# Kernel optimization log

Measured on AMD Instinct MI355X. Metric: run time of the kernel, lower is better.

Reference implementation:

```python
import jax, jax.numpy as jnp
import numpy as np

B, T, D, H = 2, 2048, 2048, 32
d = D // H  # head_dim = 64


def setup_inputs() -> dict:
    key = jax.random.key(0)
    ks = jax.random.split(key, 6)
    s = 2 ** (-2.5) * (2.0 / (D + D)) ** 0.5  # xavier_uniform-ish scale, gain 2^-2.5
    return {
        "hidden_states": jax.random.normal(ks[0], (B, T, D), jnp.float32),
        "Wq": jax.random.normal(ks[1], (D, D), jnp.float32) * s,
        "Wk": jax.random.normal(ks[2], (D, D), jnp.float32) * s,
        "Wv": jax.random.normal(ks[3], (D, D), jnp.float32) * s,
        "Wbeta": jax.random.normal(ks[4], (D, H), jnp.float32) * s,
        "b_beta": jnp.zeros((H,), jnp.float32),
        "Wo": jax.random.normal(ks[5], (D, D), jnp.float32) * s,
    }


def _l2norm(x):
    return x * jax.lax.rsqrt(jnp.sum(x * x, axis=-1, keepdims=True) + 1e-6)


def _parallel_hope(q, k, v, beta):
    """Householder delta-rule linear attention.
    q,k,v: [B,H,T,d]; beta: [B,H,T].
    Recurrence: S_t = S_{t-1} (I - beta_t k_t k_t^T) + beta_t k_t v_t^T  (k l2-normalized,
    so the update is a generalized Householder transform), o_t = q_t^T S_t.
    """
    q = _l2norm(q)
    k = _l2norm(k)

    def step(S, inp):
        q_t, k_t, v_t, b_t = inp  # [B,H,d], [B,H,d], [B,H,d], [B,H]
        # delta rule: new value replaces old prediction, gated by beta
        pred = jnp.einsum('bhk,bhkv->bhv', k_t, S)
        delta = (v_t - pred) * b_t[..., None]
        S = S + jnp.einsum('bhk,bhv->bhkv', k_t, delta)
        o_t = jnp.einsum('bhk,bhkv->bhv', q_t, S)
        return S, o_t

    S0 = jnp.zeros(q.shape[:2] + (q.shape[-1], v.shape[-1]), q.dtype)  # [B,H,d,d]
    xs = (jnp.moveaxis(q, 2, 0), jnp.moveaxis(k, 2, 0),
          jnp.moveaxis(v, 2, 0), jnp.moveaxis(beta, 2, 0))
    _, o = jax.lax.scan(step, S0, xs)  # [T,B,H,d]
    return jnp.moveaxis(o, 0, 2)  # [B,H,T,d]


def reference(hidden_states, Wq, Wk, Wv, Wbeta, b_beta, Wo):
    q = hidden_states @ Wq
    k = hidden_states @ Wk
    v = hidden_states @ Wv
    beta = jax.nn.sigmoid(hidden_states @ Wbeta + b_beta)  # [B,T,H]
    to_heads = lambda x: jnp.moveaxis(x.reshape(B, T, H, d), 1, 2)  # [B,H,T,d]
    q, k, v = to_heads(q), to_heads(k), to_heads(v)
    beta = jnp.moveaxis(beta, 1, 2)  # [B,H,T]
    o = _parallel_hope(q, k, v, beta)  # [B,H,T,d]
    o = jnp.moveaxis(o, 1, 2).reshape(B, T, D)
    return o @ Wo
```

## Files before the change

kernel.cpp:

```cpp
#include <hip/hip_runtime.h>
#include <hip/hip_bf16.h>

typedef __hip_bfloat16 bf16;
typedef __attribute__((ext_vector_type(8))) short short8;
typedef __attribute__((ext_vector_type(4))) float f32x4;

#define NB 2
#define NT 2048
#define ND 2048
#define NH 32
#define NM (NB*NT)
#define NCH 32

__global__ void detect_dtype(const unsigned short* __restrict__ hs, int* __restrict__ flag) {
  if (threadIdx.x == 0 && blockIdx.x == 0) {
    int cnt = 0;
    for (int i = 0; i < 2048; i += 2) {
      int e = (hs[i] >> 7) & 0xFF;
      if (e >= 141) ++cnt;
    }
    *flag = (cnt > 64) ? 1 : 0;
  }
}

__device__ __forceinline__ float loadf(const void* p, size_t i, int isf32) {
  return isf32 ? ((const float*)p)[i] : __bfloat162float(((const bf16*)p)[i]);
}

__global__ __launch_bounds__(256) void convert_bf16(const void* __restrict__ src,
                                                    bf16* __restrict__ dst,
                                                    long n, const int* __restrict__ flag) {
  const long i0 = ((long)blockIdx.x * 256 + threadIdx.x) * 8;
  if (i0 >= n) return;
  if (*flag) {
    const float* s = (const float*)src;
    #pragma unroll
    for (int j = 0; j < 8; ++j) dst[i0 + j] = __float2bfloat16(s[i0 + j]);
  } else {
    *(short8*)(dst + i0) = *(const short8*)((const bf16*)src + i0);
  }
}

__global__ __launch_bounds__(256) void transpose_cvt(const void* __restrict__ src,
                                                     bf16* __restrict__ dst,
                                                     int src_rows, int src_cols,
                                                     const int* __restrict__ flag) {
  __shared__ bf16 tile[64][65];
  const int f = *flag;
  const int tb_r = blockIdx.y * 64, tb_c = blockIdx.x * 64;
  const int tx = threadIdx.x & 63, ty = threadIdx.x >> 6;
  #pragma unroll
  for (int i = 0; i < 64; i += 4) {
    const int cc = tb_c + tx;
    tile[i + ty][tx] = (cc < src_cols)
      ? __float2bfloat16(loadf(src, (size_t)(tb_r + i + ty) * src_cols + cc, f))
      : __float2bfloat16(0.f);
  }
  __syncthreads();
  #pragma unroll
  for (int i = 0; i < 64; i += 4)
    dst[(size_t)(tb_c + i + ty) * src_rows + tb_r + tx] = tile[tx][i + ty];
}

__global__ __launch_bounds__(256) void transpose_qkvb(const void* __restrict__ Wq,
                                                      const void* __restrict__ Wk,
                                                      const void* __restrict__ Wv,
                                                      const void* __restrict__ Wb,
                                                      bf16* __restrict__ WT,
                                                      const int* __restrict__ flag) {
  __shared__ bf16 tile[64][65];
  const int z = blockIdx.z;
  if (z == 3 && blockIdx.x >= 4) return;
  const void* src = (z == 0) ? Wq : (z == 1) ? Wk : (z == 2) ? Wv : Wb;
  const int src_cols = (z == 3) ? 32 : 2048;
  bf16* dst = WT + (size_t)z * 2048 * 2048;
  const int f = *flag;
  const int tb_r = blockIdx.y * 64, tb_c = blockIdx.x * 64;
  const int tx = threadIdx.x & 63, ty = threadIdx.x >> 6;
  #pragma unroll
  for (int i = 0; i < 64; i += 4) {
    const int cc = tb_c + tx;
    tile[i + ty][tx] = (cc < src_cols)
      ? __float2bfloat16(loadf(src, (size_t)(tb_r + i + ty) * src_cols + cc, f))
      : __float2bfloat16(0.f);
  }
  __syncthreads();
  #pragma unroll
  for (int i = 0; i < 64; i += 4)
    dst[(size_t)(tb_c + i + ty) * 2048 + tb_r + tx] = tile[tx][i + ty];
}

__device__ __forceinline__ void gload_lds16(const void* g, void* l) {
  __builtin_amdgcn_global_load_lds((__attribute__((address_space(1))) const void*)g,
                                   (__attribute__((address_space(3))) void*)l,
                                   16, 0, 0);
}

__global__ __launch_bounds__(256) void gemm_bt(const bf16* __restrict__ A,
                                               const bf16* __restrict__ Bt,
                                               bf16* __restrict__ oq, bf16* __restrict__ ok2,
                                               bf16* __restrict__ ov, bf16* __restrict__ ob,
                                               void* __restrict__ outv,
                                               const int* __restrict__ outflag,
                                               int M, int K, int n_base) {
  __shared__ bf16 As[128 * 32];
  __shared__ bf16 Bs[128 * 32];
  const int tid = threadIdx.x;
  const int wave = tid >> 6, lane = tid & 63;
  const int m0 = blockIdx.y * 128, n0 = blockIdx.x * 128;
  const int wm = (wave >> 1) * 64, wn = (wave & 1) * 64;
  const int srow = lane >> 2, scol = (lane & 3) * 8;
  const int frow = lane & 15, fk = (lane >> 4) * 8;
  f32x4 acc[4][4] = {};

  for (int kb = 0; kb < K; kb += 32) {
    __syncthreads();
    #pragma unroll
    for (int j = 0; j < 2; ++j) {
      const int rbase = wave * 32 + j * 16;
      gload_lds16(A  + (size_t)(m0 + rbase + srow) * K + kb + scol, As + rbase * 32);
      gload_lds16(Bt + (size_t)(n0 + rbase + srow) * K + kb + scol, Bs + rbase * 32);
    }
    __syncthreads();
    short8 af[4], bfr[4];
    #pragma unroll
    for (int i = 0; i < 4; ++i)
      af[i] = *(const short8*)(As + (wm + i * 16 + frow) * 32 + fk);
    #pragma unroll
    for (int i = 0; i < 4; ++i)
      bfr[i] = *(const short8*)(Bs + (wn + i * 16 + frow) * 32 + fk);
    #pragma unroll
    for (int mi = 0; mi < 4; ++mi)
      #pragma unroll
      for (int ni = 0; ni < 4; ++ni)
        acc[mi][ni] = __builtin_amdgcn_mfma_f32_16x16x32_bf16(af[mi], bfr[ni], acc[mi][ni], 0, 0, 0);
  }

  const int crow = (lane >> 4) * 4, ccol = lane & 15;
  const int gn0 = n_base + n0;
  if (outflag) {
    const int f = *outflag;
    #pragma unroll
    for (int mi = 0; mi < 4; ++mi)
      #pragma unroll
      for (int ni = 0; ni < 4; ++ni)
        #pragma unroll
        for (int r = 0; r < 4; ++r) {
          const size_t idx = (size_t)(m0 + wm + mi * 16 + crow + r) * 2048 + gn0 + wn + ni * 16 + ccol;
          const float val = acc[mi][ni][r];
          if (f == 1) ((float*)outv)[idx] = val;
          else        ((bf16*)outv)[idx] = __float2bfloat16(val);
        }
  } else {
    const int seg = gn0 >> 11;
    bf16* o = (seg == 0) ? oq : (seg == 1) ? ok2 : (seg == 2) ? ov : ob;
    const int stride = (seg < 3) ? 2048 : 128;
    const int cb = (gn0 & 2047) + wn;
    if (seg <= 1) {
      #pragma unroll
      for (int mi = 0; mi < 4; ++mi)
        #pragma unroll
        for (int r = 0; r < 4; ++r) {
          float s = acc[mi][0][r] * acc[mi][0][r] + acc[mi][1][r] * acc[mi][1][r]
                  + acc[mi][2][r] * acc[mi][2][r] + acc[mi][3][r] * acc[mi][3][r];
          s += __shfl_xor(s, 1, 64); s += __shfl_xor(s, 2, 64);
          s += __shfl_xor(s, 4, 64); s += __shfl_xor(s, 8, 64);
          const float inv = rsqrtf(s + 1e-6f);
          #pragma unroll
          for (int ni = 0; ni < 4; ++ni) acc[mi][ni][r] *= inv;
        }
    }
    #pragma unroll
    for (int mi = 0; mi < 4; ++mi)
      #pragma unroll
      for (int ni = 0; ni < 4; ++ni)
        #pragma unroll
        for (int r = 0; r < 4; ++r)
          o[(size_t)(m0 + wm + mi * 16 + crow + r) * stride + cb + ni * 16 + ccol] =
            __float2bfloat16(acc[mi][ni][r]);
  }
}


#define MFMA_Q(MB, NB_)                                                          \
  _Pragma("unroll") for (int mi2 = 0; mi2 < 4; ++mi2) {                          \
    _Pragma("unroll") for (int ni2 = 0; ni2 < 2; ++ni2) {                        \
      acc[(MB) + mi2][(NB_) + ni2] = __builtin_amdgcn_mfma_f32_16x16x32_bf16(    \
          aF[(MB) + mi2][0], bF[ni2][0], acc[(MB) + mi2][(NB_) + ni2], 0, 0, 0); \
      acc[(MB) + mi2][(NB_) + ni2] = __builtin_amdgcn_mfma_f32_16x16x32_bf16(    \
          aF[(MB) + mi2][1], bF[ni2][1], acc[(MB) + mi2][(NB_) + ni2], 0, 0, 0); \
    } }

#define READ_B(NBASE)                                                            \
  _Pragma("unroll") for (int ni2 = 0; ni2 < 2; ++ni2)                            \
    _Pragma("unroll") for (int kk = 0; kk < 2; ++kk)                             \
      bF[ni2][kk] = *(const short8*)((const char*)lB +                           \
        (brow0 + ((NBASE) + ni2) * 16 + frow) * 128 + kk * 64 + fcol);

#define PH_OPEN() do { __builtin_amdgcn_s_barrier();                             \
  asm volatile("s_waitcnt lgkmcnt(0)" ::: "memory");                             \
  __builtin_amdgcn_sched_barrier(0);                                             \
  __builtin_amdgcn_s_setprio(1); } while (0)

#define PH_CLOSE() do { __builtin_amdgcn_s_setprio(0);                           \
  __builtin_amdgcn_s_barrier(); } while (0)

__global__ __launch_bounds__(512, 2) void gemm256(const bf16* __restrict__ A,
                                                  const bf16* __restrict__ Bt,
                                                  bf16* __restrict__ oq, bf16* __restrict__ ok2,
                                                  bf16* __restrict__ ov, bf16* __restrict__ ob,
                                                  int K, int ntn) {
  __shared__ bf16 LA[2][2][8192];
  __shared__ bf16 LB[2][2][8192];
  const int tid = threadIdx.x;
  const int wave = tid >> 6, lane = tid & 63;
  const int wm = wave >> 2, wn = wave & 3;
  const int frow = lane & 15, fq = lane >> 4;
  const int cpx = (int)gridDim.x >> 3;
  const int wg = ((int)blockIdx.x & 7) * cpx + ((int)blockIdx.x >> 3);
  const int mtile = wg / ntn, ntile = wg % ntn;
  const int m0 = mtile * 256, n0 = ntile * 256;
  const int NTK = K >> 6;
  const int fcol = (fq * 16) ^ (((frow >> 2) & 1) << 5);
  int srow[2], scolb[2];
  #pragma unroll
  for (int j = 0; j < 2; ++j) {
    const int q = wave * 1024 + j * 8192 + lane * 16;
    const int qs = q ^ (((q >> 9) & 1) << 5);
    srow[j] = qs >> 7;
    scolb[j] = (qs & 127) >> 1;
  }
  const int lofs = wave * 1024;

  f32x4 acc[8][4] = {};

  auto STAGE = [&](const bf16* __restrict__ G, int row0, int kcol, bf16* lhalf) {
    #pragma unroll
    for (int j = 0; j < 2; ++j)
      gload_lds16(G + (size_t)(row0 + srow[j]) * K + kcol + scolb[j],
                  (char*)lhalf + lofs + j * 8192);
  };

  STAGE(A,  m0,       0,  LA[0][0]);
  STAGE(A,  m0 + 128, 0,  LA[0][1]);
  STAGE(Bt, n0,       0,  LB[0][0]);
  STAGE(Bt, n0 + 128, 0,  LB[0][1]);
  STAGE(A,  m0,       64, LA[1][0]);
  STAGE(A,  m0 + 128, 64, LA[1][1]);
  asm volatile("s_waitcnt vmcnt(4)" ::: "memory");
  __builtin_amdgcn_s_barrier();

  const int brow0 = (wn & 1) * 64;
  #pragma unroll 1
  for (int t = 0; t < NTK; ++t) {
    const int par = t & 1;
    const bf16* lA = LA[par][wm];
    const bf16* lB = LB[par][wn >> 1];
    short8 aF[8][2], bF[2][2];
    #pragma unroll
    for (int mi = 0; mi < 8; ++mi)
      #pragma unroll
      for (int kk = 0; kk < 2; ++kk)
        aF[mi][kk] = *(const short8*)((const char*)lA + (mi * 16 + frow) * 128 + kk * 64 + fcol);
    READ_B(0)
    if (t + 1 < NTK) STAGE(Bt, n0, (t + 1) * 64, LB[par ^ 1][0]);
    PH_OPEN();
    MFMA_Q(0, 0)
    PH_CLOSE();
    READ_B(2)
    if (t + 1 < NTK) STAGE(Bt, n0 + 128, (t + 1) * 64, LB[par ^ 1][1]);
    if (t + 2 < NTK) STAGE(A, m0, (t + 2) * 64, LA[par][0]);
    PH_OPEN();
    MFMA_Q(0, 2)
    PH_CLOSE();
    READ_B(0)
    if (t + 2 < NTK) STAGE(A, m0 + 128, (t + 2) * 64, LA[par][1]);
    PH_OPEN();
    MFMA_Q(4, 0)
    PH_CLOSE();
    READ_B(2)
    PH_OPEN();
    MFMA_Q(4, 2)
    __builtin_amdgcn_s_setprio(0);
    if (t + 1 < NTK) {
      if (t == NTK - 2) asm volatile("s_waitcnt vmcnt(0)" ::: "memory");
      else              asm volatile("s_waitcnt vmcnt(4)" ::: "memory");
      __builtin_amdgcn_s_barrier();
    }
  }

  const int crow = fq * 4, ccol = frow;
  const int gn0w = n0 + wn * 64;
  const int seg = gn0w >> 11;
  bf16* o = (seg == 0) ? oq : (seg == 1) ? ok2 : (seg == 2) ? ov : ob;
  const int stride = (seg < 3) ? 2048 : 256;
  const int cb = (seg < 3) ? (gn0w & 2047) : (gn0w - 6144);
  if (seg <= 1) {
    #pragma unroll
    for (int mi = 0; mi < 8; ++mi)
      #pragma unroll
      for (int r = 0; r < 4; ++r) {
        float s = acc[mi][0][r] * acc[mi][0][r] + acc[mi][1][r] * acc[mi][1][r]
                + acc[mi][2][r] * acc[mi][2][r] + acc[mi][3][r] * acc[mi][3][r];
        s += __shfl_xor(s, 1, 64); s += __shfl_xor(s, 2, 64);
        s += __shfl_xor(s, 4, 64); s += __shfl_xor(s, 8, 64);
        const float inv = rsqrtf(s + 1e-6f);
        #pragma unroll
        for (int ni = 0; ni < 4; ++ni) acc[mi][ni][r] *= inv;
      }
  }
  const int rowb = m0 + wm * 128;
  #pragma unroll
  for (int mi = 0; mi < 8; ++mi)
    #pragma unroll
    for (int ni = 0; ni < 4; ++ni)
      #pragma unroll
      for (int r = 0; r < 4; ++r)
        o[(size_t)(rowb + mi * 16 + crow + r) * stride + cb + ni * 16 + ccol] =
          __float2bfloat16(acc[mi][ni][r]);
}


template<int TB>
__device__ __forceinline__ void scan16(const float* __restrict__ Af,
                                       const bf16* __restrict__ vsrc,
                                       const float* __restrict__ Bsc,
                                       float (&u)[64], const int lane, const int wave,
                                       const float sgn,
                                       bf16* __restrict__ outT,
                                       bf16* __restrict__ gout) {
  constexpr int JM = (TB + 1) * 16;
  #pragma unroll
  for (int tt = 0; tt < 16; ++tt) {
    const int t = TB * 16 + tt;
    float pr0 = 0.f, pr1 = 0.f, pr2 = 0.f, pr3 = 0.f;
    #pragma unroll
    for (int i = 0; i < JM; i += 4) {
      const f32x4 a = *(const f32x4*)(Af + t * 64 + i);
      pr0 = __builtin_fmaf(a[0], u[i + 0], pr0);
      pr1 = __builtin_fmaf(a[1], u[i + 1], pr1);
      pr2 = __builtin_fmaf(a[2], u[i + 2], pr2);
      pr3 = __builtin_fmaf(a[3], u[i + 3], pr3);
    }
    const float ut = Bsc[t] * __bfloat162float(vsrc[t * 72 + lane])
                   - ((pr0 + pr1) + (pr2 + pr3));
    u[t] = ut;
    const bf16 sv = __float2bfloat16(sgn * ut);
    outT[lane * 72 + t] = sv;
    if (wave) gout[t * 64 + lane] = sv;
  }
}

__global__ __launch_bounds__(256) void chunk_scan(const bf16* __restrict__ k16,
                                                  bf16* __restrict__ v16,
                                                  const bf16* __restrict__ betab,
                                                  const void* __restrict__ bb,
                                                  const int* __restrict__ flag,
                                                  bf16* __restrict__ Gneg,
                                                  bf16* __restrict__ AcT,
                                                  bf16* __restrict__ Dc) {
  __shared__ bf16 Ks[64 * 72];
  __shared__ bf16 Vs[64 * 72];
  __shared__ bf16 GsT[64 * 72];
  __shared__ bf16 UsT[64 * 72];
  __shared__ float Af[64 * 64];
  __shared__ float Bsc[64];
  bf16* const KTs = (bf16*)Af;
  const int ch = blockIdx.x;
  const int c = ch & (NCH - 1), bh = ch >> 5;
  const int h = bh & (NH - 1), b = bh >> 5;
  const int tid = threadIdx.x, wave = tid >> 6, lane = tid & 63;
  const size_t rowb = ((size_t)b * NT + c * 64) * ND + (size_t)h * 64;

  short8 ktA0, ktB0, ktA1, ktB1;
  if (wave >= 2) {
    const int d0a = (wave - 2) * 16, d0b = d0a + 32;
    ktA0 = *(const short8*)(k16 + rowb + (size_t)lane * ND + d0a);
    ktB0 = *(const short8*)(k16 + rowb + (size_t)lane * ND + d0a + 8);
    ktA1 = *(const short8*)(k16 + rowb + (size_t)lane * ND + d0b);
    ktB1 = *(const short8*)(k16 + rowb + (size_t)lane * ND + d0b + 8);
  }
  {
    const int r0 = tid >> 3, sc = (tid & 7) * 8;
    #pragma unroll
    for (int rnd = 0; rnd < 2; ++rnd) {
      const int r = rnd * 32 + r0;
      *(short8*)(Ks + r * 72 + sc) = *(const short8*)(k16 + rowb + (size_t)r * ND + sc);
      *(short8*)(Vs + r * 72 + sc) = *(const short8*)(v16 + rowb + (size_t)r * ND + sc);
    }
  }
  if (tid < 64) {
    const float x = __bfloat162float(betab[((size_t)b * NT + c * 64 + tid) * 256 + h])
                    + loadf(bb, h, *flag);
    Bsc[tid] = 1.f / (1.f + expf(-x));
  }
  __syncthreads();

  const int frow = lane & 15, fk = (lane >> 4) * 8, cm = (lane >> 4) * 4;
  {
    short8 ma0 = *(const short8*)(Ks + (16 * wave + frow) * 72 + fk);
    short8 ma1 = *(const short8*)(Ks + (16 * wave + frow) * 72 + 32 + fk);
    #pragma unroll
    for (int n = 0; n < 4; ++n) {
      f32x4 m = {};
      m = __builtin_amdgcn_mfma_f32_16x16x32_bf16(ma0, *(const short8*)(Ks + (16 * n + frow) * 72 + fk), m, 0, 0, 0);
      m = __builtin_amdgcn_mfma_f32_16x16x32_bf16(ma1, *(const short8*)(Ks + (16 * n + frow) * 72 + 32 + fk), m, 0, 0, 0);
      #pragma unroll
      for (int r = 0; r < 4; ++r) {
        const int t = 16 * wave + cm + r, s = 16 * n + frow;
        Af[t * 64 + s] = (s < t) ? Bsc[t] * m[r] : 0.f;
      }
    }
  }
  __syncthreads();

  if (wave < 2) {
    float u[64];
    #pragma unroll
    for (int i = 0; i < 64; ++i) u[i] = 0.f;
    const bf16* vsrc = wave ? Ks : Vs;
    bf16* outT = wave ? GsT : UsT;
    bf16* gout = Gneg + (size_t)ch * 4096;
    const float sgn = wave ? -1.f : 1.f;
    scan16<0>(Af, vsrc, Bsc, u, lane, wave, sgn, outT, gout);
    scan16<1>(Af, vsrc, Bsc, u, lane, wave, sgn, outT, gout);
    scan16<2>(Af, vsrc, Bsc, u, lane, wave, sgn, outT, gout);
    scan16<3>(Af, vsrc, Bsc, u, lane, wave, sgn, outT, gout);
  }
  __syncthreads();

  if (wave >= 2) {
    const int d0a = (wave - 2) * 16, d0b = d0a + 32;
    #pragma unroll
    for (int j = 0; j < 8; ++j) {
      KTs[(d0a + j) * 72 + lane]     = ((const bf16*)&ktA0)[j];
      KTs[(d0a + 8 + j) * 72 + lane] = ((const bf16*)&ktB0)[j];
      KTs[(d0b + j) * 72 + lane]     = ((const bf16*)&ktA1)[j];
      KTs[(d0b + 8 + j) * 72 + lane] = ((const bf16*)&ktB1)[j];
    }
  }
  __syncthreads();

  short8 ka0 = *(const short8*)(KTs + (16 * wave + frow) * 72 + fk);
  short8 ka1 = *(const short8*)(KTs + (16 * wave + frow) * 72 + 32 + fk);
  short8 uu0 = *(const short8*)(UsT + (16 * wave + frow) * 72 + fk);
  short8 uu1 = *(const short8*)(UsT + (16 * wave + frow) * 72 + 32 + fk);
  #pragma unroll
  for (int n = 0; n < 4; ++n) {
    f32x4 aA = {}, aD = {};
    aA = __builtin_amdgcn_mfma_f32_16x16x32_bf16(ka0, *(const short8*)(GsT + (16 * n + frow) * 72 + fk), aA, 0, 0, 0);
    aA = __builtin_amdgcn_mfma_f32_16x16x32_bf16(ka1, *(const short8*)(GsT + (16 * n + frow) * 72 + 32 + fk), aA, 0, 0, 0);
    aD = __builtin_amdgcn_mfma_f32_16x16x32_bf16(uu0, *(const short8*)(KTs + (16 * n + frow) * 72 + fk), aD, 0, 0, 0);
    aD = __builtin_amdgcn_mfma_f32_16x16x32_bf16(uu1, *(const short8*)(KTs + (16 * n + frow) * 72 + 32 + fk), aD, 0, 0, 0);
    #pragma unroll
    for (int r = 0; r < 4; ++r) {
      Vs[(16 * wave + cm + r) * 64 + 16 * n + frow] = __float2bfloat16(aA[r]);
      Ks[(16 * wave + cm + r) * 64 + 16 * n + frow] = __float2bfloat16(aD[r]);
    }
  }
  __syncthreads();
  {
    const int r0 = tid >> 2, sc2 = (tid & 3) * 16;
    bf16* acg = AcT + (size_t)ch * 4096;
    bf16* dcg = Dc  + (size_t)ch * 4096;
    *(short8*)(acg + r0 * 64 + sc2)     = *(const short8*)(Vs + r0 * 64 + sc2);
    *(short8*)(acg + r0 * 64 + sc2 + 8) = *(const short8*)(Vs + r0 * 64 + sc2 + 8);
    *(short8*)(dcg + r0 * 64 + sc2)     = *(const short8*)(Ks + r0 * 64 + sc2);
    *(short8*)(dcg + r0 * 64 + sc2 + 8) = *(const short8*)(Ks + r0 * 64 + sc2 + 8);
    *(short8*)(v16 + rowb + (size_t)r0 * ND + sc2)     = *(const short8*)(UsT + r0 * 72 + sc2);
    *(short8*)(v16 + rowb + (size_t)r0 * ND + sc2 + 8) = *(const short8*)(UsT + r0 * 72 + sc2 + 8);
  }
}

__global__ __launch_bounds__(256) void state_seq(const bf16* __restrict__ AcT,
                                                 const bf16* __restrict__ Dc,
                                                 bf16* __restrict__ Sbuf) {
  __shared__ bf16 ST[64 * 72];
  const int bh = blockIdx.x;
  const int wave = threadIdx.x >> 6, lane = threadIdx.x & 63;
  const int frow = lane & 15, fk = (lane >> 4) * 8, cm = (lane >> 4) * 4;
  for (int i = threadIdx.x; i < 64 * 72 / 2; i += 256) ((unsigned int*)ST)[i] = 0u;
  f32x4 sacc[4] = {};
  const bf16* ac = AcT + (size_t)bh * NCH * 4096;
  const bf16* dc = Dc  + (size_t)bh * NCH * 4096;
  bf16* sb = Sbuf + (size_t)bh * NCH * 4096;
  #pragma unroll
  for (int n = 0; n < 4; ++n)
    #pragma unroll
    for (int r = 0; r < 4; ++r)
      sb[(16 * wave + cm + r) * 64 + 16 * n + frow] = __float2bfloat16(0.f);
  short8 bpre[4][2];
  float dpre[16];
  #pragma unroll
  for (int n = 0; n < 4; ++n) {
    bpre[n][0] = *(const short8*)(ac + (16 * n + frow) * 64 + fk);
    bpre[n][1] = *(const short8*)(ac + (16 * n + frow) * 64 + 32 + fk);
    #pragma unroll
    for (int r = 0; r < 4; ++r)
      dpre[n * 4 + r] = __bfloat162float(dc[(16 * wave + cm + r) * 64 + 16 * n + frow]);
  }
  __syncthreads();
  #pragma unroll 1
  for (int c = 0; c < NCH; ++c) {
    short8 a0 = *(const short8*)(ST + (16 * wave + frow) * 72 + fk);
    short8 a1 = *(const short8*)(ST + (16 * wave + frow) * 72 + 32 + fk);
    short8 bcur[4][2];
    float dcur[16];
    #pragma unroll
    for (int n = 0; n < 4; ++n) {
      bcur[n][0] = bpre[n][0]; bcur[n][1] = bpre[n][1];
      #pragma unroll
      for (int r = 0; r < 4; ++r) dcur[n * 4 + r] = dpre[n * 4 + r];
    }
    if (c + 1 < NCH) {
      const bf16* acn = ac + (size_t)(c + 1) * 4096;
      const bf16* dcn = dc + (size_t)(c + 1) * 4096;
      #pragma unroll
      for (int n = 0; n < 4; ++n) {
        bpre[n][0] = *(const short8*)(acn + (16 * n + frow) * 64 + fk);
        bpre[n][1] = *(const short8*)(acn + (16 * n + frow) * 64 + 32 + fk);
        #pragma unroll
        for (int r = 0; r < 4; ++r)
          dpre[n * 4 + r] = __bfloat162float(dcn[(16 * wave + cm + r) * 64 + 16 * n + frow]);
      }
    }
    #pragma unroll
    for (int n = 0; n < 4; ++n) {
      sacc[n] = __builtin_amdgcn_mfma_f32_16x16x32_bf16(a0, bcur[n][0], sacc[n], 0, 0, 0);
      sacc[n] = __builtin_amdgcn_mfma_f32_16x16x32_bf16(a1, bcur[n][1], sacc[n], 0, 0, 0);
      #pragma unroll
      for (int r = 0; r < 4; ++r) sacc[n][r] += dcur[n * 4 + r];
    }
    __syncthreads();
    #pragma unroll
    for (int n = 0; n < 4; ++n)
      #pragma unroll
      for (int r = 0; r < 4; ++r) {
        const bf16 sv = __float2bfloat16(sacc[n][r]);
        ST[(16 * wave + cm + r) * 72 + 16 * n + frow] = sv;
        if (c + 1 < NCH)
          sb[(size_t)(c + 1) * 4096 + (16 * wave + cm + r) * 64 + 16 * n + frow] = sv;
      }
    __syncthreads();
  }
}

__global__ __launch_bounds__(256) void chunk_out(bf16* __restrict__ q16,
                                                 const bf16* __restrict__ k16,
                                                 const bf16* __restrict__ v16,
                                                 const bf16* __restrict__ Gneg,
                                                 const bf16* __restrict__ Sbuf) {
  __shared__ bf16 UTs[64 * 72];
  __shared__ bf16 Pt[64 * 72];
  const int ch = blockIdx.x;
  const int c = ch & (NCH - 1), bh = ch >> 5;
  const int h = bh & (NH - 1), b = bh >> 5;
  const int tid = threadIdx.x, wave = tid >> 6, lane = tid & 63;
  const int frow = lane & 15, fk = (lane >> 4) * 8, cm = (lane >> 4) * 4;
  const size_t qkb = ((size_t)b * NT + c * 64) * ND + (size_t)h * 64;
  const bf16* Sb = Sbuf + (size_t)ch * 4096;
  const bf16* Gc = Gneg + (size_t)ch * 4096;
  {
    const int r0 = tid >> 2, sc2 = (tid & 3) * 16;
    *(short8*)(UTs + r0 * 72 + sc2)     = *(const short8*)(v16 + qkb + (size_t)r0 * ND + sc2);
    *(short8*)(UTs + r0 * 72 + sc2 + 8) = *(const short8*)(v16 + qkb + (size_t)r0 * ND + sc2 + 8);
  }
  short8 qa0 = *(const short8*)(q16 + qkb + (size_t)(16 * wave + frow) * ND + fk);
  short8 qa1 = *(const short8*)(q16 + qkb + (size_t)(16 * wave + frow) * ND + 32 + fk);
  f32x4 pacc[4];
  #pragma unroll
  for (int n = 0; n < 4; ++n) {
    f32x4 a = {};
    a = __builtin_amdgcn_mfma_f32_16x16x32_bf16(qa0, *(const short8*)(k16 + qkb + (size_t)(16 * n + frow) * ND + fk), a, 0, 0, 0);
    a = __builtin_amdgcn_mfma_f32_16x16x32_bf16(qa1, *(const short8*)(k16 + qkb + (size_t)(16 * n + frow) * ND + 32 + fk), a, 0, 0, 0);
    pacc[n] = a;
  }
  __syncthreads();
  f32x4 uacc[4];
  #pragma unroll
  for (int n = 0; n < 4; ++n)
    #pragma unroll
    for (int r = 0; r < 4; ++r)
      uacc[n][r] = __bfloat162float(UTs[(16 * wave + cm + r) * 72 + 16 * n + frow]);
  #pragma unroll
  for (int n = 0; n < 4; ++n)
    #pragma unroll
    for (int r = 0; r < 4; ++r) {
      const int mg = 16 * wave + cm + r, ng = 16 * n + frow;
      Pt[mg * 72 + ng] = __float2bfloat16(ng <= mg ? pacc[n][r] : 0.f);
    }
  short8 sa0 = *(const short8*)(Sb + (16 * wave + frow) * 64 + fk);
  short8 sa1 = *(const short8*)(Sb + (16 * wave + frow) * 64 + 32 + fk);
  #pragma unroll
  for (int n = 0; n < 4; ++n) {
    uacc[n] = __builtin_amdgcn_mfma_f32_16x16x32_bf16(sa0, *(const short8*)(Gc + (16 * n + frow) * 64 + fk), uacc[n], 0, 0, 0);
    uacc[n] = __builtin_amdgcn_mfma_f32_16x16x32_bf16(sa1, *(const short8*)(Gc + (16 * n + frow) * 64 + 32 + fk), uacc[n], 0, 0, 0);
  }
  __syncthreads();
  #pragma unroll
  for (int n = 0; n < 4; ++n)
    #pragma unroll
    for (int r = 0; r < 4; ++r)
      UTs[(16 * wave + cm + r) * 72 + 16 * n + frow] = __float2bfloat16(uacc[n][r]);
  __syncthreads();
  short8 pa0 = *(const short8*)(Pt + (16 * wave + frow) * 72 + fk);
  short8 pa1 = *(const short8*)(Pt + (16 * wave + frow) * 72 + 32 + fk);
  #pragma unroll
  for (int n = 0; n < 4; ++n) {
    f32x4 o = {};
    o = __builtin_amdgcn_mfma_f32_16x16x32_bf16(qa0, *(const short8*)(Sb + (16 * n + frow) * 64 + fk), o, 0, 0, 0);
    o = __builtin_amdgcn_mfma_f32_16x16x32_bf16(qa1, *(const short8*)(Sb + (16 * n + frow) * 64 + 32 + fk), o, 0, 0, 0);
    o = __builtin_amdgcn_mfma_f32_16x16x32_bf16(pa0, *(const short8*)(UTs + (16 * n + frow) * 72 + fk), o, 0, 0, 0);
    o = __builtin_amdgcn_mfma_f32_16x16x32_bf16(pa1, *(const short8*)(UTs + (16 * n + frow) * 72 + 32 + fk), o, 0, 0, 0);
    #pragma unroll
    for (int r = 0; r < 4; ++r)
      q16[qkb + (size_t)(16 * wave + cm + r) * ND + 16 * n + frow] = __float2bfloat16(o[r]);
  }
}


__global__ __launch_bounds__(128) void chunk_scan_c(const bf16* __restrict__ k16,
                                                    bf16* __restrict__ v16,
                                                    const bf16* __restrict__ betab,
                                                    const void* __restrict__ bb,
                                                    const int* __restrict__ flag,
                                                    bf16* __restrict__ Gneg) {
  __shared__ bf16 Ks[64 * 64];
  __shared__ bf16 Vs[64 * 64];
  __shared__ bf16 Gs[64 * 64];
  __shared__ float Bs[64];
  const int ch = blockIdx.x;
  const int c = ch & (NCH - 1), bh = ch >> 5;
  const int h = bh & (NH - 1), b = bh >> 5;
  const int tid = threadIdx.x;
  const int wave = tid >> 6, lane = tid & 63;
  const size_t rowb = ((size_t)b * NT + c * 64) * ND + (size_t)h * 64;
  const int sr = tid >> 3, sc = (tid & 7) * 8;
  #pragma unroll
  for (int rnd = 0; rnd < 4; ++rnd) {
    const int r = rnd * 16 + sr;
    *(short8*)(Ks + r * 64 + sc) = *(const short8*)(k16 + rowb + (size_t)r * ND + sc);
    *(short8*)(Vs + r * 64 + sc) = *(const short8*)(v16 + rowb + (size_t)r * ND + sc);
  }
  if (tid < 64) {
    const float x = __bfloat162float(betab[((size_t)b * NT + c * 64 + tid) * 128 + h])
                    + loadf(bb, h, *flag);
    Bs[tid] = 1.f / (1.f + expf(-x));
  }
  __syncthreads();
  float S[64];
  #pragma unroll
  for (int i = 0; i < 64; ++i) S[i] = 0.f;
  const bf16* val_src = wave ? Ks : Vs;
  #pragma unroll 1
  for (int t = 0; t < 64; ++t) {
    uint4 ku[8];
    #pragma unroll
    for (int i = 0; i < 8; ++i) ku[i] = ((const uint4*)(Ks + t * 64))[i];
    const float val = __bfloat162float(val_src[t * 64 + lane]);
    const float bt = Bs[t];
    float kvf[64];
    #pragma unroll
    for (int i = 0; i < 8; ++i) {
      kvf[8*i+0] = __uint_as_float(ku[i].x << 16);
      kvf[8*i+1] = __uint_as_float(ku[i].x & 0xffff0000u);
      kvf[8*i+2] = __uint_as_float(ku[i].y << 16);
      kvf[8*i+3] = __uint_as_float(ku[i].y & 0xffff0000u);
      kvf[8*i+4] = __uint_as_float(ku[i].z << 16);
      kvf[8*i+5] = __uint_as_float(ku[i].z & 0xffff0000u);
      kvf[8*i+6] = __uint_as_float(ku[i].w << 16);
      kvf[8*i+7] = __uint_as_float(ku[i].w & 0xffff0000u);
    }
    float p0 = 0, p1 = 0, p2 = 0, p3 = 0;
    #pragma unroll
    for (int i = 0; i < 16; ++i) {
      p0 += kvf[4*i+0] * S[4*i+0];
      p1 += kvf[4*i+1] * S[4*i+1];
      p2 += kvf[4*i+2] * S[4*i+2];
      p3 += kvf[4*i+3] * S[4*i+3];
    }
    const float u = bt * (val - ((p0 + p1) + (p2 + p3)));
    #pragma unroll
    for (int i = 0; i < 16; ++i) {
      S[4*i+0] += kvf[4*i+0] * u;
      S[4*i+1] += kvf[4*i+1] * u;
      S[4*i+2] += kvf[4*i+2] * u;
      S[4*i+3] += kvf[4*i+3] * u;
    }
    if (wave) Gs[t * 64 + lane] = __float2bfloat16(-u);
    else      Vs[t * 64 + lane] = __float2bfloat16(u);
  }
  __syncthreads();
  bf16* gout = Gneg + (size_t)ch * 4096;
  #pragma unroll
  for (int rnd = 0; rnd < 4; ++rnd) {
    const int r = rnd * 16 + sr;
    *(short8*)(v16 + rowb + (size_t)r * ND + sc) = *(const short8*)(Vs + r * 64 + sc);
    *(short8*)(gout + r * 64 + sc)               = *(const short8*)(Gs + r * 64 + sc);
  }
}

__global__ __launch_bounds__(256) void chunk_seq_mono(bf16* q16,
                                                      const bf16* __restrict__ k16,
                                                      const bf16* __restrict__ Ul,
                                                      const bf16* __restrict__ Gneg) {
  __shared__ bf16 ST[64 * 72];
  __shared__ bf16 Ubt[64 * 72];
  __shared__ bf16 Pt[64 * 72];
  __shared__ bf16 KTl[64 * 72];
  const int bh = blockIdx.x, h = bh & (NH - 1), b = bh >> 5;
  const int wave = threadIdx.x >> 6, lane = threadIdx.x & 63;
  const int frow = lane & 15, q4 = lane >> 4, fk = q4 * 8;
  const int cm = q4 * 4;
  for (int i = threadIdx.x; i < 64 * 72 / 2; i += 256) ((unsigned int*)ST)[i] = 0u;
  __syncthreads();
  f32x4 sacc[4] = {};
  #pragma unroll 1
  for (int c = 0; c < NCH; ++c) {
    const bf16* Gc = Gneg + ((size_t)bh * NCH + c) * 4096;
    const size_t qkb = ((size_t)b * NT + c * 64) * ND + (size_t)h * 64;
    {
      short8 r0 = *(const short8*)(k16 + qkb + (size_t)lane * ND + 16 * wave);
      short8 r1 = *(const short8*)(k16 + qkb + (size_t)lane * ND + 16 * wave + 8);
      #pragma unroll
      for (int j = 0; j < 8; ++j) {
        KTl[(16 * wave + j) * 72 + lane]     = ((const bf16*)&r0)[j];
        KTl[(16 * wave + 8 + j) * 72 + lane] = ((const bf16*)&r1)[j];
      }
    }
    short8 ga0 = *(const short8*)(Gc + (16 * wave + frow) * 64 + fk);
    short8 ga1 = *(const short8*)(Gc + (16 * wave + frow) * 64 + 32 + fk);
    #pragma unroll
    for (int n = 0; n < 4; ++n) {
      f32x4 acc;
      #pragma unroll
      for (int r = 0; r < 4; ++r)
        acc[r] = __bfloat162float(Ul[qkb + (size_t)(16 * wave + cm + r) * ND + 16 * n + frow]);
      acc = __builtin_amdgcn_mfma_f32_16x16x32_bf16(ga0, *(const short8*)(ST + (16 * n + frow) * 72 + fk), acc, 0, 0, 0);
      acc = __builtin_amdgcn_mfma_f32_16x16x32_bf16(ga1, *(const short8*)(ST + (16 * n + frow) * 72 + 32 + fk), acc, 0, 0, 0);
      #pragma unroll
      for (int r = 0; r < 4; ++r)
        Ubt[(16 * n + frow) * 72 + 16 * wave + cm + r] = __float2bfloat16(acc[r]);
    }
    __syncthreads();
    short8 qa0 = *(const short8*)(q16 + qkb + (size_t)(16 * wave + frow) * ND + fk);
    short8 qa1 = *(const short8*)(q16 + qkb + (size_t)(16 * wave + frow) * ND + 32 + fk);
    #pragma unroll
    for (int n = 0; n < 4; ++n) {
      f32x4 acc = {};
      acc = __builtin_amdgcn_mfma_f32_16x16x32_bf16(qa0, *(const short8*)(k16 + qkb + (size_t)(16 * n + frow) * ND + fk), acc, 0, 0, 0);
      acc = __builtin_amdgcn_mfma_f32_16x16x32_bf16(qa1, *(const short8*)(k16 + qkb + (size_t)(16 * n + frow) * ND + 32 + fk), acc, 0, 0, 0);
      #pragma unroll
      for (int r = 0; r < 4; ++r) {
        const int mg = 16 * wave + cm + r, ng = 16 * n + frow;
        Pt[mg * 72 + ng] = __float2bfloat16(ng <= mg ? acc[r] : 0.f);
      }
    }
    __syncthreads();
    short8 pa0 = *(const short8*)(Pt + (16 * wave + frow) * 72 + fk);
    short8 pa1 = *(const short8*)(Pt + (16 * wave + frow) * 72 + 32 + fk);
    #pragma unroll
    for (int n = 0; n < 4; ++n) {
      f32x4 acc = {};
      acc = __builtin_amdgcn_mfma_f32_16x16x32_bf16(qa0, *(const short8*)(ST + (16 * n + frow) * 72 + fk), acc, 0, 0, 0);
      acc = __builtin_amdgcn_mfma_f32_16x16x32_bf16(qa1, *(const short8*)(ST + (16 * n + frow) * 72 + 32 + fk), acc, 0, 0, 0);
      acc = __builtin_amdgcn_mfma_f32_16x16x32_bf16(pa0, *(const short8*)(Ubt + (16 * n + frow) * 72 + fk), acc, 0, 0, 0);
      acc = __builtin_amdgcn_mfma_f32_16x16x32_bf16(pa1, *(const short8*)(Ubt + (16 * n + frow) * 72 + 32 + fk), acc, 0, 0, 0);
      #pragma unroll
      for (int r = 0; r < 4; ++r)
        q16[qkb + (size_t)(16 * wave + cm + r) * ND + 16 * n + frow] = __float2bfloat16(acc[r]);
    }
    __syncthreads();
    short8 ua0 = *(const short8*)(Ubt + (16 * wave + frow) * 72 + fk);
    short8 ua1 = *(const short8*)(Ubt + (16 * wave + frow) * 72 + 32 + fk);
    #pragma unroll
    for (int n = 0; n < 4; ++n) {
      sacc[n] = __builtin_amdgcn_mfma_f32_16x16x32_bf16(ua0, *(const short8*)(KTl + (16 * n + frow) * 72 + fk), sacc[n], 0, 0, 0);
      sacc[n] = __builtin_amdgcn_mfma_f32_16x16x32_bf16(ua1, *(const short8*)(KTl + (16 * n + frow) * 72 + 32 + fk), sacc[n], 0, 0, 0);
      #pragma unroll
      for (int r = 0; r < 4; ++r)
        ST[(16 * wave + cm + r) * 72 + 16 * n + frow] = __float2bfloat16(sacc[n][r]);
    }
    __syncthreads();
  }
}

extern "C" void kernel_launch(void* const* d_in, const int* in_sizes, int n_in,
                              void* d_out, int out_size, void* d_ws, size_t ws_size,
                              hipStream_t stream) {
  const void* hs = d_in[0];
  const void* Wq = d_in[1];
  const void* Wk = d_in[2];
  const void* Wv = d_in[3];
  const void* Wb = d_in[4];
  const void* bb = d_in[5];
  const void* Wo = d_in[6];

  char* ws = (char*)d_ws;
  size_t off = 0;
  auto alloc = [&](size_t bytes) {
    void* p = ws + off;
    off += (bytes + 255) & ~(size_t)255;
    return p;
  };
  const size_t szW2 = (size_t)32 * 1024 * 1024;
  const size_t szM  = (size_t)NM * ND * 2;
  const size_t szB2 = (size_t)NM * 256 * 2;
  const size_t szB  = (size_t)NM * 128 * 2;
  const size_t need_fused = 512 + szW2 + 4 * szM + szB2 + szM;

  if (ws_size >= need_fused) {
    int*  flag  = (int*) alloc(256);
    bf16* WT    = (bf16*)alloc(szW2);
    bf16* hs16  = (bf16*)alloc(szM);
    bf16* q16   = (bf16*)alloc(szM);
    bf16* k16   = (bf16*)alloc(szM);
    bf16* v16   = (bf16*)alloc(szM);
    bf16* betab = (bf16*)alloc(szB2);
    bf16* Dc    = (bf16*)alloc(szM);
    bf16* Gneg  = WT;
    bf16* AcT   = WT + (size_t)8 * 1024 * 1024;
    bf16* WoT   = AcT;
    bf16* Sbuf  = hs16;

    detect_dtype<<<1, 64, 0, stream>>>((const unsigned short*)hs, flag);
    convert_bf16<<<(NM * ND) / (256 * 8), 256, 0, stream>>>(hs, hs16, (long)NM * ND, flag);

    transpose_qkvb<<<dim3(32, 32, 4), 256, 0, stream>>>(Wq, Wk, Wv, Wb, WT, flag);
    gemm256<<<400, 512, 0, stream>>>(hs16, WT, q16, k16, v16, betab, ND, 25);

    chunk_scan<<<NB * NH * NCH, 256, 0, stream>>>(k16, v16, betab, bb, flag, Gneg, AcT, Dc);
    state_seq<<<NB * NH, 256, 0, stream>>>(AcT, Dc, Sbuf);
    chunk_out<<<NB * NH * NCH, 256, 0, stream>>>(q16, k16, v16, Gneg, Sbuf);

    transpose_cvt<<<dim3(32, 32), 256, 0, stream>>>(Wo, WoT, 2048, 2048, flag);
    gemm_bt<<<dim3(16, 32), 256, 0, stream>>>(q16, WoT, nullptr, nullptr, nullptr, nullptr,
                                              d_out, flag, NM, ND, 0);
  } else {
    int*  flag  = (int*) alloc(256);
    bf16* Wt    = (bf16*)alloc((size_t)2048 * 2048 * 2);
    bf16* hs16  = (bf16*)alloc(szM);
    bf16* q16   = (bf16*)alloc(szM);
    bf16* k16   = (bf16*)alloc(szM);
    bf16* v16   = (bf16*)alloc(szM);
    bf16* betab = (bf16*)alloc(szB);
    bf16* Gneg  = hs16;

    detect_dtype<<<1, 64, 0, stream>>>((const unsigned short*)hs, flag);
    convert_bf16<<<(NM * ND) / (256 * 8), 256, 0, stream>>>(hs, hs16, (long)NM * ND, flag);

    transpose_cvt<<<dim3(32, 32), 256, 0, stream>>>(Wq, Wt, 2048, 2048, flag);
    gemm_bt<<<dim3(16, 32), 256, 0, stream>>>(hs16, Wt, q16, k16, v16, betab, nullptr, nullptr, NM, ND, 0);
    transpose_cvt<<<dim3(32, 32), 256, 0, stream>>>(Wk, Wt, 2048, 2048, flag);
    gemm_bt<<<dim3(16, 32), 256, 0, stream>>>(hs16, Wt, q16, k16, v16, betab, nullptr, nullptr, NM, ND, 2048);
    transpose_cvt<<<dim3(32, 32), 256, 0, stream>>>(Wv, Wt, 2048, 2048, flag);
    gemm_bt<<<dim3(16, 32), 256, 0, stream>>>(hs16, Wt, q16, k16, v16, betab, nullptr, nullptr, NM, ND, 4096);
    transpose_cvt<<<dim3(2, 32),  256, 0, stream>>>(Wb, Wt, 2048, 32, flag);
    gemm_bt<<<dim3(1, 32), 256, 0, stream>>>(hs16, Wt, q16, k16, v16, betab, nullptr, nullptr, NM, ND, 6144);

    chunk_scan_c<<<NB * NH * NCH, 128, 0, stream>>>(k16, v16, betab, bb, flag, Gneg);
    chunk_seq_mono<<<NB * NH, 256, 0, stream>>>(q16, k16, v16, Gneg);

    transpose_cvt<<<dim3(32, 32), 256, 0, stream>>>(Wo, Wt, 2048, 2048, flag);
    gemm_bt<<<dim3(16, 32), 256, 0, stream>>>(q16, Wt, nullptr, nullptr, nullptr, nullptr,
                                              d_out, flag, NM, ND, 0);
  }
}
```

Baseline: 588.7 us.

## Restructure gemm256 fragment loop, widen LDS swizzle, reuse it for output projection

```diff
diff --git a/kernel.cpp b/kernel.cpp
--- a/kernel.cpp
+++ b/kernel.cpp
@@ -182,20 +182,26 @@
 }
 
 
-#define MFMA_Q(MB, NB_)                                                          \
-  _Pragma("unroll") for (int mi2 = 0; mi2 < 4; ++mi2) {                          \
-    _Pragma("unroll") for (int ni2 = 0; ni2 < 2; ++ni2) {                        \
-      acc[(MB) + mi2][(NB_) + ni2] = __builtin_amdgcn_mfma_f32_16x16x32_bf16(    \
-          aF[(MB) + mi2][0], bF[ni2][0], acc[(MB) + mi2][(NB_) + ni2], 0, 0, 0); \
-      acc[(MB) + mi2][(NB_) + ni2] = __builtin_amdgcn_mfma_f32_16x16x32_bf16(    \
-          aF[(MB) + mi2][1], bF[ni2][1], acc[(MB) + mi2][(NB_) + ni2], 0, 0, 0); \
-    } }
-
-#define READ_B(NBASE)                                                            \
-  _Pragma("unroll") for (int ni2 = 0; ni2 < 2; ++ni2)                            \
+#define MFMA_PAIR(P)                                                             \
+  _Pragma("unroll") for (int q2 = 0; q2 < 2; ++q2)                               \
+    _Pragma("unroll") for (int ni2 = 0; ni2 < 4; ++ni2) {                        \
+      acc[(P) * 2 + q2][ni2] = __builtin_amdgcn_mfma_f32_16x16x32_bf16(          \
+          aF[q2][0], bF[ni2][0], acc[(P) * 2 + q2][ni2], 0, 0, 0);               \
+      acc[(P) * 2 + q2][ni2] = __builtin_amdgcn_mfma_f32_16x16x32_bf16(          \
+          aF[q2][1], bF[ni2][1], acc[(P) * 2 + q2][ni2], 0, 0, 0);               \
+    }
+
+#define READ_A(P)                                                                \
+  _Pragma("unroll") for (int q2 = 0; q2 < 2; ++q2)                               \
     _Pragma("unroll") for (int kk = 0; kk < 2; ++kk)                             \
-      bF[ni2][kk] = *(const short8*)((const char*)lB +                           \
-        (brow0 + ((NBASE) + ni2) * 16 + frow) * 128 + kk * 64 + fcol);
+      aF[q2][kk] = *(const short8*)(lA + (((P) * 2 + q2) * 16 + frow) * 128      \
+                                       + ((kk * 64 + fq * 16) ^ fswz));
+
+#define READ_B_ALL()                                                             \
+  _Pragma("unroll") for (int ni2 = 0; ni2 < 4; ++ni2)                            \
+    _Pragma("unroll") for (int kk = 0; kk < 2; ++kk)                             \
+      bF[ni2][kk] = *(const short8*)(lB + (brow0 + ni2 * 16 + frow) * 128        \
+                                        + ((kk * 64 + fq * 16) ^ fswz));
 
 #define PH_OPEN() do { __builtin_amdgcn_s_barrier();                             \
   asm volatile("s_waitcnt lgkmcnt(0)" ::: "memory");                             \
@@ -209,6 +215,8 @@
                                                   const bf16* __restrict__ Bt,
                                                   bf16* __restrict__ oq, bf16* __restrict__ ok2,
                                                   bf16* __restrict__ ov, bf16* __restrict__ ob,
+                                                  void* __restrict__ outv,
+                                                  const int* __restrict__ outflag,
                                                   int K, int ntn) {
   __shared__ bf16 LA[2][2][8192];
   __shared__ bf16 LB[2][2][8192];
@@ -221,13 +229,13 @@
   const int mtile = wg / ntn, ntile = wg % ntn;
   const int m0 = mtile * 256, n0 = ntile * 256;
   const int NTK = K >> 6;
-  const int fcol = (fq * 16) ^ (((frow >> 2) & 1) << 5);
+  const int fswz = (frow & 7) << 4;
   int srow[2], scolb[2];
   #pragma unroll
   for (int j = 0; j < 2; ++j) {
     const int q = wave * 1024 + j * 8192 + lane * 16;
-    const int qs = q ^ (((q >> 9) & 1) << 5);
-    srow[j] = qs >> 7;
+    const int qs = q ^ (((q >> 7) & 7) << 4);
+    srow[j]  = qs >> 7;
     scolb[j] = (qs & 127) >> 1;
   }
   const int lofs = wave * 1024;
@@ -254,35 +262,34 @@
   #pragma unroll 1
   for (int t = 0; t < NTK; ++t) {
     const int par = t & 1;
-    const bf16* lA = LA[par][wm];
-    const bf16* lB = LB[par][wn >> 1];
-    short8 aF[8][2], bF[2][2];
-    #pragma unroll
-    for (int mi = 0; mi < 8; ++mi)
-      #pragma unroll
-      for (int kk = 0; kk < 2; ++kk)
-        aF[mi][kk] = *(const short8*)((const char*)lA + (mi * 16 + frow) * 128 + kk * 64 + fcol);
-    READ_B(0)
+    const char* lA = (const char*)LA[par][wm];
+    const char* lB = (const char*)LB[par][wn >> 1];
+    short8 aF[2][2], bF[4][2];
+    READ_A(0)
+    READ_B_ALL()
     if (t + 1 < NTK) STAGE(Bt, n0, (t + 1) * 64, LB[par ^ 1][0]);
     PH_OPEN();
-    MFMA_Q(0, 0)
+    MFMA_PAIR(0)
     PH_CLOSE();
-    READ_B(2)
+    READ_A(1)
     if (t + 1 < NTK) STAGE(Bt, n0 + 128, (t + 1) * 64, LB[par ^ 1][1]);
-    if (t + 2 < NTK) STAGE(A, m0, (t + 2) * 64, LA[par][0]);
     PH_OPEN();
-    MFMA_Q(0, 2)
+    MFMA_PAIR(1)
     PH_CLOSE();
-    READ_B(0)
-    if (t + 2 < NTK) STAGE(A, m0 + 128, (t + 2) * 64, LA[par][1]);
+    READ_A(2)
     PH_OPEN();
-    MFMA_Q(4, 0)
+    MFMA_PAIR(2)
     PH_CLOSE();
-    READ_B(2)
+    READ_A(3)
     PH_OPEN();
-    MFMA_Q(4, 2)
+    MFMA_PAIR(3)
     __builtin_amdgcn_s_setprio(0);
+    __builtin_amdgcn_s_barrier();
     if (t + 1 < NTK) {
+      if (t + 2 < NTK) {
+        STAGE(A, m0,       (t + 2) * 64, LA[par][0]);
+        STAGE(A, m0 + 128, (t + 2) * 64, LA[par][1]);
+      }
       if (t == NTK - 2) asm volatile("s_waitcnt vmcnt(0)" ::: "memory");
       else              asm volatile("s_waitcnt vmcnt(4)" ::: "memory");
       __builtin_amdgcn_s_barrier();
@@ -290,6 +297,23 @@
   }
 
   const int crow = fq * 4, ccol = frow;
+  const int rowb = m0 + wm * 128;
+  if (outv) {
+    const int f = *outflag;
+    const int cb = n0 + wn * 64;
+    #pragma unroll
+    for (int mi = 0; mi < 8; ++mi)
+      #pragma unroll
+      for (int ni = 0; ni < 4; ++ni)
+        #pragma unroll
+        for (int r = 0; r < 4; ++r) {
+          const size_t idx = (size_t)(rowb + mi * 16 + crow + r) * 2048 + cb + ni * 16 + ccol;
+          const float val = acc[mi][ni][r];
+          if (f == 1) ((float*)outv)[idx] = val;
+          else        ((bf16*)outv)[idx] = __float2bfloat16(val);
+        }
+    return;
+  }
   const int gn0w = n0 + wn * 64;
   const int seg = gn0w >> 11;
   bf16* o = (seg == 0) ? oq : (seg == 1) ? ok2 : (seg == 2) ? ov : ob;
@@ -309,7 +333,6 @@
         for (int ni = 0; ni < 4; ++ni) acc[mi][ni][r] *= inv;
       }
   }
-  const int rowb = m0 + wm * 128;
   #pragma unroll
   for (int mi = 0; mi < 8; ++mi)
     #pragma unroll
@@ -827,15 +850,16 @@
     convert_bf16<<<(NM * ND) / (256 * 8), 256, 0, stream>>>(hs, hs16, (long)NM * ND, flag);
 
     transpose_qkvb<<<dim3(32, 32, 4), 256, 0, stream>>>(Wq, Wk, Wv, Wb, WT, flag);
-    gemm256<<<400, 512, 0, stream>>>(hs16, WT, q16, k16, v16, betab, ND, 25);
+    gemm256<<<400, 512, 0, stream>>>(hs16, WT, q16, k16, v16, betab,
+                                     nullptr, nullptr, ND, 25);
 
     chunk_scan<<<NB * NH * NCH, 256, 0, stream>>>(k16, v16, betab, bb, flag, Gneg, AcT, Dc);
     state_seq<<<NB * NH, 256, 0, stream>>>(AcT, Dc, Sbuf);
     chunk_out<<<NB * NH * NCH, 256, 0, stream>>>(q16, k16, v16, Gneg, Sbuf);
 
     transpose_cvt<<<dim3(32, 32), 256, 0, stream>>>(Wo, WoT, 2048, 2048, flag);
-    gemm_bt<<<dim3(16, 32), 256, 0, stream>>>(q16, WoT, nullptr, nullptr, nullptr, nullptr,
-                                              d_out, flag, NM, ND, 0);
+    gemm256<<<128, 512, 0, stream>>>(q16, WoT, nullptr, nullptr, nullptr, nullptr,
+                                     d_out, flag, ND, 8);
   } else {
     int*  flag  = (int*) alloc(256);
     bf16* Wt    = (bf16*)alloc((size_t)2048 * 2048 * 2);
```

Result: no change. 581.8 us (-1.2%).
